# Performance work log

Measured on AMD Instinct MI355X. Metric: run time of the kernel, lower is better.

The kernel has to match this reference:

```python
import jax, jax.numpy as jnp
import numpy as np

EMBED_DIM = 1024
NUM_HEADS = 16
HEAD_DIM = EMBED_DIM // NUM_HEADS


def setup_inputs() -> dict:
    key = jax.random.key(0)
    ks = jax.random.split(key, 9)
    B, S, E, hd = 2, 2048, EMBED_DIM, HEAD_DIM
    s_e = 1.0 / np.sqrt(E)
    return {
        "x": jax.random.normal(ks[0], (B, S, E), dtype=jnp.float32),
        "wq": jax.random.uniform(ks[1], (E, E), jnp.float32, -s_e, s_e),
        "bq": jax.random.uniform(ks[2], (E,), jnp.float32, -s_e, s_e),
        "wk": jax.random.uniform(ks[3], (E, hd), jnp.float32, -s_e, s_e),
        "bk": jax.random.uniform(ks[4], (hd,), jnp.float32, -s_e, s_e),
        "wv": jax.random.uniform(ks[5], (E, hd), jnp.float32, -s_e, s_e),
        "bv": jax.random.uniform(ks[6], (hd,), jnp.float32, -s_e, s_e),
        "wo": jax.random.uniform(ks[7], (E, E), jnp.float32, -s_e, s_e),
        "bo": jax.random.uniform(ks[8], (E,), jnp.float32, -s_e, s_e),
    }


def reference(x, wq, bq, wk, bk, wv, bv, wo, bo):
    B, S, E = x.shape
    H, hd = NUM_HEADS, HEAD_DIM
    # projections
    q = (x @ wq + bq).reshape(B, S, H, hd)          # [B,S,H,hd]
    k = x @ wk + bk                                  # [B,S,hd] shared across heads
    v = x @ wv + bv                                  # [B,S,hd]
    scale = 1.0 / np.sqrt(hd).astype(np.float32)
    # scores: [B,H,S_q,S_k]
    scores = jnp.einsum('bqhd,bkd->bhqk', q, k) * scale
    attn = jax.nn.softmax(scores, axis=-1)
    out = jnp.einsum('bhqk,bkd->bqhd', attn, v).reshape(B, S, E)
    return out @ wo + bo
```

## Files before the change

### kernel.cpp

```cpp
#include <hip/hip_runtime.h>
#include <stdint.h>

#define SLEN 2048
#define EDIM 1024
#define NH 16
#define HD 64
#define QLD 1152
#define NSPLIT 2

typedef unsigned short u16;
typedef short bf8 __attribute__((ext_vector_type(8)));
typedef float f4 __attribute__((ext_vector_type(4)));
typedef float f16f __attribute__((ext_vector_type(16)));
typedef int v2i __attribute__((ext_vector_type(2)));
typedef bf8 bf8_a __attribute__((may_alias));
typedef uint2 uint2_a __attribute__((may_alias));
typedef uint4 uint4_a __attribute__((may_alias));

__device__ __forceinline__ float bf2f(u16 u) {
  union { unsigned u; float f; } c; c.u = ((unsigned)u) << 16; return c.f;
}
__device__ __forceinline__ u16 f2bf(float x) {
  union { __bf16 h; u16 u; } c; c.h = (__bf16)x; return c.u;
}
__device__ __forceinline__ unsigned pk2bf(float a, float b) {
  union { __bf16 h[2]; unsigned u; } c;
  c.h[0] = (__bf16)a; c.h[1] = (__bf16)b;
  return c.u;
}
__device__ __forceinline__ void async_cp16(u16* lds, const u16* g) {
  __builtin_amdgcn_global_load_lds((__attribute__((address_space(1))) void*)g,
                                   (__attribute__((address_space(3))) void*)lds,
                                   16, 0, 0);
}

__device__ __forceinline__ void tcvt_tile(const float* src, int srcLd,
                                          u16* dst, int dstLd, int r0, int c0) {
  __shared__ u16 tile[64][65];
  const int t = threadIdx.x;
#pragma unroll
  for (int i = 0; i < 16; ++i) {
    int e = i * 256 + t, rr = e >> 6, cc = e & 63;
    tile[rr][cc] = f2bf(src[(size_t)(r0 + rr) * srcLd + c0 + cc]);
  }
  __syncthreads();
#pragma unroll
  for (int i = 0; i < 16; ++i) {
    int e = i * 256 + t, j = e >> 6, ii = e & 63;
    dst[(size_t)(c0 + j) * dstLd + r0 + ii] = tile[ii][j];
  }
}

__global__ void prep_w(const float* wq, const float* wk, const float* wv,
                       const float* wo, const float* bq, const float* bk,
                       const float* bv, const float* bo, const float* x,
                       u16* wT, u16* woT, float* bQKV, float* bOut, u16* xbf) {
  const int yy = blockIdx.y;
  if (yy < 16) tcvt_tile(wq, 1024, wT, 1024, blockIdx.x * 64, yy * 64);
  else if (yy < 32) tcvt_tile(wo, 1024, woT, 1024, blockIdx.x * 64, (yy - 16) * 64);
  else if (yy == 32) tcvt_tile(wk, 64, wT + (size_t)1024 * 1024, 1024, blockIdx.x * 64, 0);
  else if (yy == 33) tcvt_tile(wv, 64, wT + (size_t)1088 * 1024, 1024, blockIdx.x * 64, 0);
  else if (yy == 34) {
    int i = blockIdx.x * 256 + threadIdx.x;
    if (i < 1024) bQKV[i] = bq[i];
    else if (i < 1088) bQKV[i] = bk[i - 1024];
    else if (i < 1152) bQKV[i] = bv[i - 1088];
    int j = i - 1152;
    if (j >= 0 && j < 1024) bOut[j] = bo[j];
  } else {
    const int blk = (yy - 35) * 16 + blockIdx.x, t = threadIdx.x;
#pragma unroll
    for (int i = 0; i < 8; ++i) {
      int idx = blk * 16384 + i * 2048 + t * 8;
      u16 tmp[8];
#pragma unroll
      for (int j = 0; j < 8; ++j) tmp[j] = f2bf(x[idx + j]);
      *(uint4_a*)&xbf[idx] = *(const uint4_a*)tmp;
    }
  }
}

__global__ __launch_bounds__(256) void gemm_bt_bias(
    const u16* __restrict__ A, const u16* __restrict__ Bt,
    const float* __restrict__ bias, void* __restrict__ C, int K, int ldc,
    int ofp32, u16* __restrict__ vtb) {
  __shared__ __align__(16) u16 As[64 * 64];
  __shared__ __align__(16) u16 Bs[128 * 64];
  const int tn0 = blockIdx.x * 128, tm0 = blockIdx.y * 64;
  const int tid = threadIdx.x, wave = tid >> 6, lane = tid & 63;
  const int quad = lane >> 4, l16 = lane & 15;
  const int wm = wave & 1, wn = wave >> 1;

  f4 acc[2][4];
#pragma unroll
  for (int i = 0; i < 2; ++i)
#pragma unroll
    for (int j = 0; j < 4; ++j) acc[i][j] = f4{0.f, 0.f, 0.f, 0.f};

  int aslot[2], bslot[4]; size_t aoff[2], boff[4];
#pragma unroll
  for (int i = 0; i < 2; ++i) {
    int s = i * 256 + tid, m = s >> 3, kc = s & 7, c = (kc - m) & 7;
    aslot[i] = s; aoff[i] = (size_t)(tm0 + m) * K + c * 8;
  }
#pragma unroll
  for (int i = 0; i < 4; ++i) {
    int s = i * 256 + tid, n = s >> 3, kc = s & 7, c = (kc - n) & 7;
    bslot[i] = s; boff[i] = (size_t)(tn0 + n) * K + c * 8;
  }
  int ard[2][2], brd[4][2];
#pragma unroll
  for (int mi = 0; mi < 2; ++mi) {
    int m = wm * 32 + mi * 16 + l16;
#pragma unroll
    for (int kk = 0; kk < 2; ++kk)
      ard[mi][kk] = (m * 8 + (((kk * 4 + quad) + m) & 7)) * 8;
  }
#pragma unroll
  for (int ni = 0; ni < 4; ++ni) {
    int n = wn * 64 + ni * 16 + l16;
#pragma unroll
    for (int kk = 0; kk < 2; ++kk)
      brd[ni][kk] = (n * 8 + (((kk * 4 + quad) + n) & 7)) * 8;
  }

  const int kIt = K >> 6;
  for (int it = 0; it < kIt; ++it) {
    __syncthreads();
    const size_t kb = (size_t)it * 64;
#pragma unroll
    for (int i = 0; i < 2; ++i) async_cp16(&As[aslot[i] * 8], A + aoff[i] + kb);
#pragma unroll
    for (int i = 0; i < 4; ++i) async_cp16(&Bs[bslot[i] * 8], Bt + boff[i] + kb);
    __syncthreads();
#pragma unroll
    for (int kk = 0; kk < 2; ++kk) {
      bf8 af[2], bfr[4];
#pragma unroll
      for (int mi = 0; mi < 2; ++mi) af[mi] = *(const bf8_a*)&As[ard[mi][kk]];
#pragma unroll
      for (int ni = 0; ni < 4; ++ni) bfr[ni] = *(const bf8_a*)&Bs[brd[ni][kk]];
#pragma unroll
      for (int mi = 0; mi < 2; ++mi)
#pragma unroll
        for (int ni = 0; ni < 4; ++ni)
          acc[mi][ni] = __builtin_amdgcn_mfma_f32_16x16x32_bf16(
              af[mi], bfr[ni], acc[mi][ni], 0, 0, 0);
    }
  }

  const float QSCALE = 0.125f * 1.44269504089f;
  float bv[4];
#pragma unroll
  for (int ni = 0; ni < 4; ++ni) bv[ni] = bias[tn0 + wn * 64 + ni * 16 + l16];
#pragma unroll
  for (int mi = 0; mi < 2; ++mi) {
    int row0 = tm0 + wm * 32 + mi * 16 + quad * 4;
#pragma unroll
    for (int ni = 0; ni < 4; ++ni) {
      int col = tn0 + wn * 64 + ni * 16 + l16;
      float vv[4];
#pragma unroll
      for (int r = 0; r < 4; ++r) vv[r] = acc[mi][ni][r] + bv[ni];
      if (vtb != nullptr && col < 1024) {
#pragma unroll
        for (int r = 0; r < 4; ++r) vv[r] *= QSCALE;
      }
      if (ofp32) {
#pragma unroll
        for (int r = 0; r < 4; ++r)
          ((float*)C)[(size_t)(row0 + r) * ldc + col] = vv[r];
      } else {
#pragma unroll
        for (int r = 0; r < 4; ++r)
          ((u16*)C)[(size_t)(row0 + r) * ldc + col] = f2bf(vv[r]);
      }
      if (vtb != nullptr && col >= 1088) {
        int d = col - 1088, bb = row0 >> 11, s0 = row0 & 2047;
        uint2 pk;
        pk.x = pk2bf(vv[0], vv[1]);
        pk.y = pk2bf(vv[2], vv[3]);
        *(uint2_a*)&vtb[(size_t)(bb * 64 + d) * SLEN + s0] = pk;
      }
    }
  }
}

__global__ __launch_bounds__(256, 2) void attn_kernel(
    const u16* __restrict__ qkv, const u16* __restrict__ vT,
    u16* __restrict__ Opart, float* __restrict__ lpart) {
  __shared__ __align__(16) u16 Kf[2][8192];
  __shared__ __align__(16) u16 Vf[2][8192];
  const int qt = blockIdx.x, bh = blockIdx.y, ks = blockIdx.z;
  const int b = bh >> 4, h = bh & 15;
  const int tid = threadIdx.x, wave = tid >> 6, lane = tid & 63;
  const int l31 = lane & 31, hi = lane >> 5, r16l = lane & 15;
  const int base_k = (l31 >> 4) * 64 + hi * 16 + r16l;

  u16* Kflat = &Kf[0][0];
#pragma unroll
  for (int i = 0; i < 8; ++i) {
    int d = i * 256 + tid;
    int sel = d >> 10, dl = d & 1023;
    int kk = dl >> 9, g = (dl >> 6) & 7, qd = (dl >> 4) & 3, r16 = dl & 15;
    async_cp16(&Kflat[(sel * 1024 + dl) * 8],
               qkv + (size_t)(b * SLEN + qt * 256 + sel * 128 + g * 16 + r16) * QLD +
                   h * HD + (kk * 4 + qd) * 8);
  }
  __syncthreads();
  bf8 bq[2][4];
  {
    const u16* srcf = Kflat + (wave >> 1) * 8192;
#pragma unroll
    for (int qset = 0; qset < 2; ++qset) {
      int gq = (wave & 1) * 2 + qset;
#pragma unroll
      for (int kk2 = 0; kk2 < 4; ++kk2) {
        int c = base_k + gq * 128 + (kk2 >> 1) * 512 + (kk2 & 1) * 32;
        bq[qset][kk2] = *(const bf8_a*)&srcf[c * 8];
      }
    }
  }
  __syncthreads();

  const int kbase = ks * (SLEN / NSPLIT);
  const u16* kp[2]; const u16* vp[2];
#pragma unroll
  for (int i = 0; i < 2; ++i) {
    int d = i * 256 + tid;
    int kk = d >> 8, k8 = (d >> 6) & 3, qd = (d >> 4) & 3, r16 = d & 15;
    kp[i] = qkv + (size_t)(b * SLEN + kbase + k8 * 16 + r16) * QLD + EDIM +
            (kk * 4 + qd) * 8;
    int k4 = d >> 8, ni = (d >> 6) & 3;
    vp[i] = vT + (size_t)(b * 64 + ni * 16 + r16) * SLEN + kbase +
            (k4 * 4 + qd) * 8;
  }
  auto stage = [&](int bsel) {
#pragma unroll
    for (int s = 0; s < 2; ++s)
#pragma unroll
      for (int i = 0; i < 2; ++i) {
        int d = i * 256 + tid;
        async_cp16(&Kf[bsel][s * 4096 + d * 8], kp[i] + s * 64 * QLD);
        async_cp16(&Vf[bsel][s * 4096 + d * 8], vp[i] + s * 64);
      }
#pragma unroll
    for (int i = 0; i < 2; ++i) { kp[i] += 128 * QLD; vp[i] += 128; }
  };
  stage(0);

  f16f acc_o[2][2];
#pragma unroll
  for (int qset = 0; qset < 2; ++qset)
#pragma unroll
    for (int i = 0; i < 2; ++i)
#pragma unroll
      for (int r = 0; r < 16; ++r) acc_o[qset][i][r] = 0.f;
  f4 lracc[2] = {f4{0.f, 0.f, 0.f, 0.f}, f4{0.f, 0.f, 0.f, 0.f}};

  const int NHALF = SLEN / NSPLIT / 128;
  for (int hh = 0; hh < NHALF; ++hh) {
    __syncthreads();
    if (hh < NHALF - 1) stage((hh + 1) & 1);
    const int bsel = hh & 1;

#pragma unroll
    for (int sub = 0; sub < 2; ++sub) {
      const u16* kf = &Kf[bsel][sub * 4096];
      const u16* vf = &Vf[bsel][sub * 4096];

#pragma unroll
      for (int j32 = 0; j32 < 2; ++j32) {
        f16f st0, st1;
#pragma unroll
        for (int r = 0; r < 16; ++r) { st0[r] = 0.f; st1[r] = 0.f; }
        __builtin_amdgcn_s_setprio(1);
#pragma unroll
        for (int kk2 = 0; kk2 < 4; ++kk2) {
          bf8 ak = *(const bf8_a*)
              &kf[(base_k + (kk2 >> 1) * 256 + j32 * 128 + (kk2 & 1) * 32) * 8];
          st0 = __builtin_amdgcn_mfma_f32_32x32x16_bf16(ak, bq[0][kk2], st0, 0, 0, 0);
          st1 = __builtin_amdgcn_mfma_f32_32x32x16_bf16(ak, bq[1][kk2], st1, 0, 0, 0);
        }
        __builtin_amdgcn_s_setprio(0);

        bf8 pa[2][2];
#pragma unroll
        for (int qset = 0; qset < 2; ++qset) {
          float pe[16];
#pragma unroll
          for (int r = 0; r < 16; ++r) {
            pe[r] = __builtin_amdgcn_exp2f(qset ? st1[r] : st0[r]);
            lracc[qset][r & 3] += pe[r];
          }
          int a0 = (int)pk2bf(pe[0], pe[1]),   b0 = (int)pk2bf(pe[4], pe[5]);
          int a1 = (int)pk2bf(pe[2], pe[3]),   b1 = (int)pk2bf(pe[6], pe[7]);
          int a2 = (int)pk2bf(pe[8], pe[9]),   b2 = (int)pk2bf(pe[12], pe[13]);
          int a3 = (int)pk2bf(pe[10], pe[11]), b3 = (int)pk2bf(pe[14], pe[15]);
          v2i s0 = __builtin_amdgcn_permlane32_swap(a0, b0, false, false);
          v2i s1 = __builtin_amdgcn_permlane32_swap(a1, b1, false, false);
          v2i s2 = __builtin_amdgcn_permlane32_swap(a2, b2, false, false);
          v2i s3 = __builtin_amdgcn_permlane32_swap(a3, b3, false, false);
          union { int i[4]; bf8 v; } up0, up1;
          up0.i[0] = s0[0]; up0.i[1] = s1[0]; up0.i[2] = s0[1]; up0.i[3] = s1[1];
          up1.i[0] = s2[0]; up1.i[1] = s3[0]; up1.i[2] = s2[1]; up1.i[3] = s3[1];
          pa[qset][0] = up0.v;
          pa[qset][1] = up1.v;
        }

        __builtin_amdgcn_s_setprio(1);
#pragma unroll
        for (int ks2 = 0; ks2 < 2; ++ks2)
#pragma unroll
          for (int ni2 = 0; ni2 < 2; ++ni2) {
            bf8 bv = *(const bf8_a*)
                &vf[(base_k + j32 * 256 + ni2 * 128 + ks2 * 32) * 8];
            acc_o[0][ni2] = __builtin_amdgcn_mfma_f32_32x32x16_bf16(
                pa[0][ks2], bv, acc_o[0][ni2], 0, 0, 0);
            acc_o[1][ni2] = __builtin_amdgcn_mfma_f32_32x32x16_bf16(
                pa[1][ks2], bv, acc_o[1][ni2], 0, 0, 0);
          }
        __builtin_amdgcn_s_setprio(0);
      }
    }
  }

  const size_t pbase = (size_t)((ks * 32 + bh) * 8 + qt) * 256;
#pragma unroll
  for (int qset = 0; qset < 2; ++qset) {
    float lr = (lracc[qset][0] + lracc[qset][1]) + (lracc[qset][2] + lracc[qset][3]);
    float s = lr + __shfl_xor(lr, 32, 64);
    if (lane < 32) lpart[pbase + wave * 64 + qset * 32 + lane] = s;
  }
#pragma unroll
  for (int qset = 0; qset < 2; ++qset)
#pragma unroll
    for (int ni2 = 0; ni2 < 2; ++ni2)
#pragma unroll
      for (int r = 0; r < 16; ++r) {
        int q = (r & 3) + 8 * (r >> 2) + 4 * hi;
        Opart[(pbase + wave * 64 + qset * 32 + q) * 64 + ni2 * 32 + l31] =
            f2bf(acc_o[qset][ni2][r]);
      }
}

__global__ __launch_bounds__(256) void reduce_o(const u16* __restrict__ Op,
                                                const float* __restrict__ lp,
                                                u16* __restrict__ aob) {
  const int qt = blockIdx.x, bh = blockIdx.y, b = bh >> 4, h = bh & 15;
  const int t = threadIdx.x, r = t >> 1, dh = (t & 1) * 32;
  const int g = qt * 128 + r;
  const int blk = g >> 8, loc = g & 255;
  size_t p[NSPLIT];
#pragma unroll
  for (int i = 0; i < NSPLIT; ++i)
    p[i] = (size_t)((i * 32 + bh) * 8 + blk) * 256 + loc;
  float lsum = 0.f;
#pragma unroll
  for (int i = 0; i < NSPLIT; ++i) lsum += lp[p[i]];
  const float inv = 1.f / lsum;
  u16* dst = aob + (size_t)(b * SLEN + g) * EDIM + h * HD + dh;
#pragma unroll
  for (int c = 0; c < 4; ++c) {
    float accv[8] = {0.f, 0.f, 0.f, 0.f, 0.f, 0.f, 0.f, 0.f};
#pragma unroll
    for (int i = 0; i < NSPLIT; ++i) {
      uint4 a = *(const uint4_a*)(Op + p[i] * 64 + dh + c * 8);
      const u16* pa = (const u16*)&a;
#pragma unroll
      for (int j = 0; j < 8; ++j) accv[j] += bf2f(pa[j]);
    }
    u16 outv[8];
#pragma unroll
    for (int j = 0; j < 8; ++j) outv[j] = f2bf(accv[j] * inv);
    *(uint4_a*)(dst + c * 8) = *(const uint4_a*)outv;
  }
}

extern "C" void kernel_launch(void* const* d_in, const int* in_sizes, int n_in,
                              void* d_out, int out_size, void* d_ws, size_t ws_size,
                              hipStream_t stream) {
  const float* x  = (const float*)d_in[0];
  const float* wq = (const float*)d_in[1];
  const float* bq = (const float*)d_in[2];
  const float* wk = (const float*)d_in[3];
  const float* bk = (const float*)d_in[4];
  const float* wv = (const float*)d_in[5];
  const float* bv = (const float*)d_in[6];
  const float* wo = (const float*)d_in[7];
  const float* bo = (const float*)d_in[8];

  char* ws = (char*)d_ws;
  size_t off = 0;
  auto carve = [&](size_t bytes) {
    void* p = ws + off;
    off = (off + bytes + 255) & ~(size_t)255;
    return p;
  };
  u16* wT      = (u16*)carve((size_t)1152 * 1024 * 2);
  u16* woT     = (u16*)carve((size_t)1024 * 1024 * 2);
  float* bQKV  = (float*)carve(1152 * 4);
  float* bOut  = (float*)carve(1024 * 4);
  u16* xbf     = (u16*)carve((size_t)4096 * EDIM * 2);
  u16* qkvb    = (u16*)carve((size_t)4096 * QLD * 2);
  u16* vTb     = (u16*)carve((size_t)2 * 64 * SLEN * 2);
  u16* Opart   = (u16*)carve((size_t)NSPLIT * 32 * 8 * 256 * 64 * 2);
  float* lpart = (float*)carve((size_t)NSPLIT * 32 * 8 * 256 * 4);
  u16* aob     = (u16*)carve((size_t)4096 * EDIM * 2);

  prep_w<<<dim3(16, 51), 256, 0, stream>>>(wq, wk, wv, wo, bq, bk, bv, bo, x,
                                           wT, woT, bQKV, bOut, xbf);

  gemm_bt_bias<<<dim3(9, 64), 256, 0, stream>>>(xbf, wT, bQKV, qkvb, 1024, QLD,
                                                0, vTb);

  attn_kernel<<<dim3(8, 32, NSPLIT), 256, 0, stream>>>(qkvb, vTb, Opart, lpart);
  reduce_o<<<dim3(16, 32), 256, 0, stream>>>(Opart, lpart, aob);

  gemm_bt_bias<<<dim3(8, 64), 256, 0, stream>>>(aob, woT, bOut, d_out, 1024,
                                                1024, 1, nullptr);
}
```

Baseline: 180.2 us.

## Fuse split-KV partial reduction into output projection GEMM A-tile load

Removes the separate reduce_o kernel and the intermediate bf16 attention-output buffer by having the output GEMM combine the two split partials and normalize by the summed softmax denominators while loading its A tile. This saves a launch and a full write and read of the intermediate. In exchange, each column-tile block re-reads and re-reduces the partials, and the A-tile path changes from async copies to synchronous loads plus arithmetic before the LDS store.

```diff
diff --git a/kernel.cpp b/kernel.cpp
--- a/kernel.cpp
+++ b/kernel.cpp
@@ -83,7 +83,8 @@
 __global__ __launch_bounds__(256) void gemm_bt_bias(
     const u16* __restrict__ A, const u16* __restrict__ Bt,
     const float* __restrict__ bias, void* __restrict__ C, int K, int ldc,
-    int ofp32, u16* __restrict__ vtb) {
+    int ofp32, u16* __restrict__ vtb,
+    const u16* __restrict__ OpA, const float* __restrict__ lpA) {
   __shared__ __align__(16) u16 As[64 * 64];
   __shared__ __align__(16) u16 Bs[128 * 64];
   const int tn0 = blockIdx.x * 128, tm0 = blockIdx.y * 64;
@@ -98,10 +99,12 @@
     for (int j = 0; j < 4; ++j) acc[i][j] = f4{0.f, 0.f, 0.f, 0.f};
 
   int aslot[2], bslot[4]; size_t aoff[2], boff[4];
+  int am[2], ac[2];
 #pragma unroll
   for (int i = 0; i < 2; ++i) {
     int s = i * 256 + tid, m = s >> 3, kc = s & 7, c = (kc - m) & 7;
     aslot[i] = s; aoff[i] = (size_t)(tm0 + m) * K + c * 8;
+    am[i] = m; ac[i] = c;
   }
 #pragma unroll
   for (int i = 0; i < 4; ++i) {
@@ -122,14 +125,42 @@
 #pragma unroll
     for (int kk = 0; kk < 2; ++kk)
       brd[ni][kk] = (n * 8 + (((kk * 4 + quad) + n) & 7)) * 8;
+  }
+
+  size_t apbase[2]; int ablk[2];
+#pragma unroll
+  for (int i = 0; i < 2; ++i) {
+    int grow = tm0 + am[i];
+    int b = grow >> 11, g = grow & 2047;
+    ablk[i] = (b << 4);
+    apbase[i] = (size_t)(g >> 8) * 256 + (g & 255);
   }
 
   const int kIt = K >> 6;
   for (int it = 0; it < kIt; ++it) {
     __syncthreads();
     const size_t kb = (size_t)it * 64;
-#pragma unroll
-    for (int i = 0; i < 2; ++i) async_cp16(&As[aslot[i] * 8], A + aoff[i] + kb);
+    if (OpA == nullptr) {
+#pragma unroll
+      for (int i = 0; i < 2; ++i) async_cp16(&As[aslot[i] * 8], A + aoff[i] + kb);
+    } else {
+#pragma unroll
+      for (int i = 0; i < 2; ++i) {
+        int bh = ablk[i] + it;
+        size_t p0 = (size_t)(bh * 8) * 256 + apbase[i];
+        size_t p1 = (size_t)((32 + bh) * 8) * 256 + apbase[i];
+        uint4 a0 = *(const uint4_a*)(OpA + p0 * 64 + ac[i] * 8);
+        uint4 a1 = *(const uint4_a*)(OpA + p1 * 64 + ac[i] * 8);
+        float inv = 1.f / (lpA[p0] + lpA[p1]);
+        const u16* q0 = (const u16*)&a0;
+        const u16* q1 = (const u16*)&a1;
+        u16 outv[8];
+#pragma unroll
+        for (int j = 0; j < 8; ++j)
+          outv[j] = f2bf((bf2f(q0[j]) + bf2f(q1[j])) * inv);
+        *(uint4_a*)&As[aslot[i] * 8] = *(const uint4_a*)outv;
+      }
+    }
 #pragma unroll
     for (int i = 0; i < 4; ++i) async_cp16(&Bs[bslot[i] * 8], Bt + boff[i] + kb);
     __syncthreads();
@@ -344,39 +375,6 @@
       }
 }
 
-__global__ __launch_bounds__(256) void reduce_o(const u16* __restrict__ Op,
-                                                const float* __restrict__ lp,
-                                                u16* __restrict__ aob) {
-  const int qt = blockIdx.x, bh = blockIdx.y, b = bh >> 4, h = bh & 15;
-  const int t = threadIdx.x, r = t >> 1, dh = (t & 1) * 32;
-  const int g = qt * 128 + r;
-  const int blk = g >> 8, loc = g & 255;
-  size_t p[NSPLIT];
-#pragma unroll
-  for (int i = 0; i < NSPLIT; ++i)
-    p[i] = (size_t)((i * 32 + bh) * 8 + blk) * 256 + loc;
-  float lsum = 0.f;
-#pragma unroll
-  for (int i = 0; i < NSPLIT; ++i) lsum += lp[p[i]];
-  const float inv = 1.f / lsum;
-  u16* dst = aob + (size_t)(b * SLEN + g) * EDIM + h * HD + dh;
-#pragma unroll
-  for (int c = 0; c < 4; ++c) {
-    float accv[8] = {0.f, 0.f, 0.f, 0.f, 0.f, 0.f, 0.f, 0.f};
-#pragma unroll
-    for (int i = 0; i < NSPLIT; ++i) {
-      uint4 a = *(const uint4_a*)(Op + p[i] * 64 + dh + c * 8);
-      const u16* pa = (const u16*)&a;
-#pragma unroll
-      for (int j = 0; j < 8; ++j) accv[j] += bf2f(pa[j]);
-    }
-    u16 outv[8];
-#pragma unroll
-    for (int j = 0; j < 8; ++j) outv[j] = f2bf(accv[j] * inv);
-    *(uint4_a*)(dst + c * 8) = *(const uint4_a*)outv;
-  }
-}
-
 extern "C" void kernel_launch(void* const* d_in, const int* in_sizes, int n_in,
                               void* d_out, int out_size, void* d_ws, size_t ws_size,
                               hipStream_t stream) {
@@ -406,17 +404,15 @@
   u16* vTb     = (u16*)carve((size_t)2 * 64 * SLEN * 2);
   u16* Opart   = (u16*)carve((size_t)NSPLIT * 32 * 8 * 256 * 64 * 2);
   float* lpart = (float*)carve((size_t)NSPLIT * 32 * 8 * 256 * 4);
-  u16* aob     = (u16*)carve((size_t)4096 * EDIM * 2);
 
   prep_w<<<dim3(16, 51), 256, 0, stream>>>(wq, wk, wv, wo, bq, bk, bv, bo, x,
                                            wT, woT, bQKV, bOut, xbf);
 
   gemm_bt_bias<<<dim3(9, 64), 256, 0, stream>>>(xbf, wT, bQKV, qkvb, 1024, QLD,
-                                                0, vTb);
+                                                0, vTb, nullptr, nullptr);
 
   attn_kernel<<<dim3(8, 32, NSPLIT), 256, 0, stream>>>(qkvb, vTb, Opart, lpart);
-  reduce_o<<<dim3(16, 32), 256, 0, stream>>>(Opart, lpart, aob);
-
-  gemm_bt_bias<<<dim3(8, 64), 256, 0, stream>>>(aob, woT, bOut, d_out, 1024,
-                                                1024, 1, nullptr);
-}
+
+  gemm_bt_bias<<<dim3(8, 64), 256, 0, stream>>>(nullptr, woT, bOut, d_out, 1024,
+                                                1024, 1, nullptr, Opart, lpart);
+}
```

After: 185.5 us. +3.0%, slower.

## Drop split-K attention and fuse softmax normalization into attention epilogue

Applied to the files above, without the earlier changes.

Removes the two-way key split in the attention kernel so each block processes the full key sequence, and normalizes outputs by the row sum directly in the epilogue, writing into the attention-output buffer. This eliminates the partial-output and partial-sum buffers and the separate reduce kernel launch. In exchange the grid halves from 512 to 256 blocks with twice the serial loop length per block, which may reduce occupancy/parallelism on a large GPU, and the output stores are narrow scattered 2-byte writes.

```diff
diff --git a/kernel.cpp b/kernel.cpp
--- a/kernel.cpp
+++ b/kernel.cpp
@@ -6,7 +6,6 @@
 #define NH 16
 #define HD 64
 #define QLD 1152
-#define NSPLIT 2
 
 typedef unsigned short u16;
 typedef short bf8 __attribute__((ext_vector_type(8)));
@@ -188,10 +187,10 @@
 
 __global__ __launch_bounds__(256, 2) void attn_kernel(
     const u16* __restrict__ qkv, const u16* __restrict__ vT,
-    u16* __restrict__ Opart, float* __restrict__ lpart) {
+    u16* __restrict__ aob) {
   __shared__ __align__(16) u16 Kf[2][8192];
   __shared__ __align__(16) u16 Vf[2][8192];
-  const int qt = blockIdx.x, bh = blockIdx.y, ks = blockIdx.z;
+  const int qt = blockIdx.x, bh = blockIdx.y;
   const int b = bh >> 4, h = bh & 15;
   const int tid = threadIdx.x, wave = tid >> 6, lane = tid & 63;
   const int l31 = lane & 31, hi = lane >> 5, r16l = lane & 15;
@@ -223,16 +222,15 @@
   }
   __syncthreads();
 
-  const int kbase = ks * (SLEN / NSPLIT);
   const u16* kp[2]; const u16* vp[2];
 #pragma unroll
   for (int i = 0; i < 2; ++i) {
     int d = i * 256 + tid;
     int kk = d >> 8, k8 = (d >> 6) & 3, qd = (d >> 4) & 3, r16 = d & 15;
-    kp[i] = qkv + (size_t)(b * SLEN + kbase + k8 * 16 + r16) * QLD + EDIM +
+    kp[i] = qkv + (size_t)(b * SLEN + k8 * 16 + r16) * QLD + EDIM +
             (kk * 4 + qd) * 8;
     int k4 = d >> 8, ni = (d >> 6) & 3;
-    vp[i] = vT + (size_t)(b * 64 + ni * 16 + r16) * SLEN + kbase +
+    vp[i] = vT + (size_t)(b * 64 + ni * 16 + r16) * SLEN +
             (k4 * 4 + qd) * 8;
   }
   auto stage = [&](int bsel) {
@@ -258,7 +256,7 @@
       for (int r = 0; r < 16; ++r) acc_o[qset][i][r] = 0.f;
   f4 lracc[2] = {f4{0.f, 0.f, 0.f, 0.f}, f4{0.f, 0.f, 0.f, 0.f}};
 
-  const int NHALF = SLEN / NSPLIT / 128;
+  const int NHALF = SLEN / 128;
   for (int hh = 0; hh < NHALF; ++hh) {
     __syncthreads();
     if (hh < NHALF - 1) stage((hh + 1) & 1);
@@ -325,55 +323,21 @@
     }
   }
 
-  const size_t pbase = (size_t)((ks * 32 + bh) * 8 + qt) * 256;
 #pragma unroll
   for (int qset = 0; qset < 2; ++qset) {
     float lr = (lracc[qset][0] + lracc[qset][1]) + (lracc[qset][2] + lracc[qset][3]);
     float s = lr + __shfl_xor(lr, 32, 64);
-    if (lane < 32) lpart[pbase + wave * 64 + qset * 32 + lane] = s;
-  }
-#pragma unroll
-  for (int qset = 0; qset < 2; ++qset)
-#pragma unroll
-    for (int ni2 = 0; ni2 < 2; ++ni2)
-#pragma unroll
-      for (int r = 0; r < 16; ++r) {
-        int q = (r & 3) + 8 * (r >> 2) + 4 * hi;
-        Opart[(pbase + wave * 64 + qset * 32 + q) * 64 + ni2 * 32 + l31] =
-            f2bf(acc_o[qset][ni2][r]);
-      }
-}
-
-__global__ __launch_bounds__(256) void reduce_o(const u16* __restrict__ Op,
-                                                const float* __restrict__ lp,
-                                                u16* __restrict__ aob) {
-  const int qt = blockIdx.x, bh = blockIdx.y, b = bh >> 4, h = bh & 15;
-  const int t = threadIdx.x, r = t >> 1, dh = (t & 1) * 32;
-  const int g = qt * 128 + r;
-  const int blk = g >> 8, loc = g & 255;
-  size_t p[NSPLIT];
-#pragma unroll
-  for (int i = 0; i < NSPLIT; ++i)
-    p[i] = (size_t)((i * 32 + bh) * 8 + blk) * 256 + loc;
-  float lsum = 0.f;
-#pragma unroll
-  for (int i = 0; i < NSPLIT; ++i) lsum += lp[p[i]];
-  const float inv = 1.f / lsum;
-  u16* dst = aob + (size_t)(b * SLEN + g) * EDIM + h * HD + dh;
-#pragma unroll
-  for (int c = 0; c < 4; ++c) {
-    float accv[8] = {0.f, 0.f, 0.f, 0.f, 0.f, 0.f, 0.f, 0.f};
-#pragma unroll
-    for (int i = 0; i < NSPLIT; ++i) {
-      uint4 a = *(const uint4_a*)(Op + p[i] * 64 + dh + c * 8);
-      const u16* pa = (const u16*)&a;
-#pragma unroll
-      for (int j = 0; j < 8; ++j) accv[j] += bf2f(pa[j]);
-    }
-    u16 outv[8];
-#pragma unroll
-    for (int j = 0; j < 8; ++j) outv[j] = f2bf(accv[j] * inv);
-    *(uint4_a*)(dst + c * 8) = *(const uint4_a*)outv;
+    float inv = 1.f / s;
+#pragma unroll
+    for (int r = 0; r < 16; ++r) {
+      int q = (r & 3) + 8 * (r >> 2) + 4 * hi;
+      float invq = __shfl(inv, q, 64);
+      int qg = qt * 256 + wave * 64 + qset * 32 + q;
+      u16* dst = aob + (size_t)(b * SLEN + qg) * EDIM + h * HD;
+#pragma unroll
+      for (int ni2 = 0; ni2 < 2; ++ni2)
+        dst[ni2 * 32 + l31] = f2bf(acc_o[qset][ni2][r] * invq);
+    }
   }
 }
 
@@ -404,8 +368,6 @@
   u16* xbf     = (u16*)carve((size_t)4096 * EDIM * 2);
   u16* qkvb    = (u16*)carve((size_t)4096 * QLD * 2);
   u16* vTb     = (u16*)carve((size_t)2 * 64 * SLEN * 2);
-  u16* Opart   = (u16*)carve((size_t)NSPLIT * 32 * 8 * 256 * 64 * 2);
-  float* lpart = (float*)carve((size_t)NSPLIT * 32 * 8 * 256 * 4);
   u16* aob     = (u16*)carve((size_t)4096 * EDIM * 2);
 
   prep_w<<<dim3(16, 51), 256, 0, stream>>>(wq, wk, wv, wo, bq, bk, bv, bo, x,
@@ -414,8 +376,7 @@
   gemm_bt_bias<<<dim3(9, 64), 256, 0, stream>>>(xbf, wT, bQKV, qkvb, 1024, QLD,
                                                 0, vTb);
 
-  attn_kernel<<<dim3(8, 32, NSPLIT), 256, 0, stream>>>(qkvb, vTb, Opart, lpart);
-  reduce_o<<<dim3(16, 32), 256, 0, stream>>>(Opart, lpart, aob);
+  attn_kernel<<<dim3(8, 32), 256, 0, stream>>>(qkvb, vTb, aob);
 
   gemm_bt_bias<<<dim3(8, 64), 256, 0, stream>>>(aob, woT, bOut, d_out, 1024,
                                                 1024, 1, nullptr);
```

Result: no change. 183.5 us (+1.8%).
